# Performance work log

Measured on AMD Instinct MI355X. Metric: run time of the kernel, lower is better.

## Reference

```python
import jax, jax.numpy as jnp
import numpy as np
import math

B, N, A = 4, 2048, 128          # batch, natoms, neighbor_num
EMB = [1, 25, 50, 100]           # embedding net sizes (input dim 1 = S_Rij)
M = EMB[-1]
FIT = [16 * M, 240, 240, 240, 1] # fitting net sizes
RMIN, RMAX = 5.8, 6.0


def setup_inputs() -> dict:
    key = jax.random.key(0)
    ks = jax.random.split(key, 16)
    inp = {}
    inp["image_dR"] = jax.random.normal(ks[0], (B, N, A, 3), jnp.float32)
    inp["list_neigh"] = jax.random.randint(ks[1], (B, N, A), 0, N)
    ki = 2
    for i in range(3):
        inp[f"We{i}"] = jax.random.normal(ks[ki], (EMB[i], EMB[i + 1]), jnp.float32) / np.sqrt(EMB[i]).astype(np.float32)
        inp[f"be{i}"] = jnp.zeros((EMB[i + 1],), jnp.float32)
        ki += 1
    for i in range(4):
        inp[f"Wf{i}"] = jax.random.normal(ks[ki], (FIT[i], FIT[i + 1]), jnp.float32) / np.sqrt(FIT[i]).astype(np.float32)
        inp[f"bf{i}"] = jnp.zeros((FIT[i + 1],), jnp.float32)
        ki += 1
    return inp


def _forward(image_dR, list_neigh, We0, be0, We1, be1, We2, be2,
             Wf0, bf0, Wf1, bf1, Wf2, bf2, Wf3, bf3):
    # NOTE: the original assigns Rij = sqrt(dR2) then immediately overwrites
    # Rij = dR2, so all smooth/division math uses the SQUARED distance.
    Rij = jnp.sum(image_dR * image_dR, axis=-1)  # [B,N,A]
    mask = list_neigh > 0

    # smooth(): 1/x for valid & x<rmin; cosine taper for rmin<=x<rmax (unmasked,
    # exactly as in source); 0 elsewhere.
    mask_min = Rij < RMIN
    safe = jnp.where(Rij > 0, Rij, 1.0)
    s_inv = 1.0 / safe
    s_cos = 0.5 * jnp.cos(math.pi * (Rij - RMIN) / (RMAX - RMIN)) + 0.5
    S_Rij = jnp.where(mask & mask_min, s_inv,
                      jnp.where((~mask_min) & (Rij < RMAX), s_cos, 0.0))

    # The Python loop breaks at the first non-positive neighbor index, so only
    # the valid PREFIX of each neighbor list gets directional components.
    prefix = jnp.cumprod(mask.astype(jnp.int32), axis=-1).astype(bool)  # [B,N,A]
    coords = jnp.where(prefix[..., None], (S_Rij * s_inv)[..., None] * image_dR, 0.0)
    Ri = jnp.concatenate([S_Rij[..., None], coords], axis=-1)  # [B,N,A,4]

    # embedding net: S_Rij -> M channels (tanh MLP)
    h = S_Rij[..., None]
    h = jnp.tanh(h @ We0 + be0)
    h = jnp.tanh(h @ We1 + be1)
    G = jnp.tanh(h @ We2 + be2)  # [B,N,A,M]

    # tmpA = G[...,:16]^T @ Ri : [B,N,16,4];  tmpB = Ri^T @ G : [B,N,4,M]
    tmpA = jnp.einsum('bnam,bnac->bnmc', G[..., :16], Ri)
    tmpB = jnp.einsum('bnac,bnaM->bncM', Ri, G)
    DR = jnp.einsum('bnmc,bncM->bnmM', tmpA, tmpB).reshape(Ri.shape[0], Ri.shape[1], -1)  # [B,N,16*M]

    # fitting net
    h = jnp.tanh(DR @ Wf0 + bf0)
    h = jnp.tanh(h @ Wf1 + bf1)
    h = jnp.tanh(h @ Wf2 + bf2)
    Ei = h @ Wf3 + bf3          # [B,N,1]
    Etot = jnp.sum(Ei, axis=1)  # [B,1]
    return Etot, Ei


def reference(image_dR, list_neigh, We0, be0, We1, be1, We2, be2,
              Wf0, bf0, Wf1, bf1, Wf2, bf2, Wf3, bf3):
    return _forward(image_dR, list_neigh, We0, be0, We1, be1, We2, be2,
                    Wf0, bf0, Wf1, bf1, Wf2, bf2, Wf3, bf3)
```

## Files before the change

### kernel.cpp

```cpp
#include <hip/hip_runtime.h>
#include <hip/hip_bf16.h>
#include <math.h>
#include <stdint.h>

#define NB 4
#define NN 2048
#define NA 128
#define NK 2048
#define RMINF 5.8f
#define RMAXF 6.0f
#define PI_OVER_DR 15.707963267948966f

typedef __attribute__((ext_vector_type(8))) short short8v;
typedef __attribute__((ext_vector_type(4))) float f32x4;

__device__ __forceinline__ float fast_tanh(float x)
{
    x = fminf(fmaxf(x, -15.f), 15.f);
    float e = __expf(2.f * x);
    float r = __builtin_amdgcn_rcpf(e + 1.f);
    return fmaf(-2.f, r, 1.f);
}

__device__ __forceinline__ uint16_t bf16_of(float x)
{
    __hip_bfloat16 b = __float2bfloat16(x);
    return *(uint16_t*)&b;
}

__device__ __forceinline__ float bf16_to_f(uint16_t v)
{
    union { uint32_t u; float f; } c; c.u = ((uint32_t)v) << 16; return c.f;
}

__device__ __forceinline__ size_t packed_off(int r, int k, int Ktot)
{
    return ((size_t)((r >> 4) * (Ktot >> 5) + (k >> 5)) << 9)
         + (((r & 15) + (((k >> 3) & 3) << 4)) << 3) + (k & 7);
}

__device__ __forceinline__ float knot_S(int knot)
{
    float uu = (float)knot / (float)NK;
    return (knot == NK) ? 1e8f : uu / (1.f - uu);
}

__global__ void prep_h2_kernel(
    const float* __restrict__ We0, const float* __restrict__ be0,
    const float* __restrict__ We1, const float* __restrict__ be1,
    float* __restrict__ H2)
{
    int idx = blockIdx.x * 256 + threadIdx.x;
    if (idx >= (NK + 1) * 50) return;
    int knot = idx / 50, j = idx - knot * 50;
    float S = knot_S(knot);
    float acc = be1[j];
    #pragma unroll
    for (int k = 0; k < 25; ++k) {
        float h1k = fast_tanh(fmaf(S, We0[k], be0[k]));
        acc = fmaf(h1k, We1[k * 50 + j], acc);
    }
    H2[idx] = fast_tanh(acc);
}

__global__ void prep_tbl_kernel(
    const float* __restrict__ H2,
    const float* __restrict__ We2, const float* __restrict__ be2,
    float* __restrict__ TBL)
{
    int idx = blockIdx.x * 256 + threadIdx.x;
    if (idx >= (NK + 1) * 100) return;
    int knot = idx / 100, j = idx - knot * 100;
    const float* h2 = H2 + knot * 50;
    float acc = be2[j];
    #pragma unroll
    for (int k = 0; k < 50; ++k)
        acc = fmaf(h2[k], We2[k * 100 + j], acc);
    TBL[idx] = fast_tanh(acc);
}

__global__ void prep_wt_kernel(const float* __restrict__ W,
                               uint16_t* __restrict__ Whi,
                               uint16_t* __restrict__ Wlo,
                               int K, int KP)
{
    int idx = blockIdx.x * 256 + threadIdx.x;
    if (idx < 256 * KP) {
        int colN = idx / KP, k = idx - colN * KP;
        float v = (colN < 240 && k < K) ? W[k * 240 + colN] : 0.f;
        uint16_t hi = bf16_of(v);
        size_t off = packed_off(colN, k, KP);
        Whi[off] = hi;
        Wlo[off] = bf16_of(v - bf16_to_f(hi));
    }
}

__global__ __launch_bounds__(256) void desc_kernel(
    const float* __restrict__ dR, const int* __restrict__ neigh,
    const float* __restrict__ TBL,
    uint16_t* __restrict__ DRhi)
{
    const int bid = blockIdx.x;
    const int atom = (bid & 7) * 1024 + (bid >> 3);
    const int t = threadIdx.x;

    __shared__ float4 RiSh[128];
    __shared__ float2 IFSh[128];
    __shared__ float  tmpPart[8][4][100];
    __shared__ float  tmpBf[4][100];
    __shared__ unsigned long long balls[2];

    float x = 0.f, y = 0.f, z = 0.f, S = 0.f, s_inv = 1.f;
    if (t < 128) {
        const int base = atom * NA;
        x = dR[(base + t) * 3 + 0];
        y = dR[(base + t) * 3 + 1];
        z = dR[(base + t) * 3 + 2];
        int nb = neigh[base + t];
        float Rij = x * x + y * y + z * z;
        bool mask = nb > 0;
        bool mask_min = Rij < RMINF;
        float safe = (Rij > 0.f) ? Rij : 1.f;
        s_inv = 1.f / safe;
        float s_cos = 0.5f * cosf((Rij - RMINF) * PI_OVER_DR) + 0.5f;
        S = (mask && mask_min) ? s_inv
          : ((!mask_min && Rij < RMAXF) ? s_cos : 0.f);
        unsigned long long bal = __ballot(mask);
        if ((t & 63) == 0) balls[t >> 6] = bal;
    }
    __syncthreads();

    if (t < 128) {
        unsigned long long nb0 = ~balls[0], nb1 = ~balls[1];
        int firstBad;
        if (nb0)       firstBad = __ffsll((long long)nb0) - 1;
        else if (nb1)  firstBad = 64 + __ffsll((long long)nb1) - 1;
        else           firstBad = 128;
        float f = (t < firstBad) ? (S * s_inv) : 0.f;
        RiSh[t] = make_float4(S, f * x, f * y, f * z);
        float uu = S / (1.f + S);
        float pos = fminf(uu * (float)NK, (float)NK - 0.001f);
        float fi = floorf(pos);
        IFSh[t] = make_float2(pos - fi, __int_as_float((int)fi * 100));
    }
    __syncthreads();

    const int aq = t >> 5;
    const int jq = t & 31;
    if (jq < 25) {
        const float* TBLq = TBL + jq * 4;
        const int a0 = aq * 16;
        float acc00 = 0.f, acc01 = 0.f, acc02 = 0.f, acc03 = 0.f;
        float acc10 = 0.f, acc11 = 0.f, acc12 = 0.f, acc13 = 0.f;
        float acc20 = 0.f, acc21 = 0.f, acc22 = 0.f, acc23 = 0.f;
        float acc30 = 0.f, acc31 = 0.f, acc32 = 0.f, acc33 = 0.f;

        float2 ifv = IFSh[a0];
        float  cf  = ifv.x;
        int    ia  = __float_as_int(ifv.y);
        float4 t0  = *(const float4*)(TBLq + ia);
        float4 t1  = *(const float4*)(TBLq + ia + 100);
        #pragma unroll
        for (int i = 0; i < 16; ++i) {
            float g0 = fmaf(cf, t1.x - t0.x, t0.x);
            float g1 = fmaf(cf, t1.y - t0.y, t0.y);
            float g2 = fmaf(cf, t1.z - t0.z, t0.z);
            float g3 = fmaf(cf, t1.w - t0.w, t0.w);
            if (i + 1 < 16) {
                float2 nx = IFSh[a0 + i + 1];
                cf = nx.x;
                int ian = __float_as_int(nx.y);
                t0 = *(const float4*)(TBLq + ian);
                t1 = *(const float4*)(TBLq + ian + 100);
            }
            float4 cri = RiSh[a0 + i];
            acc00 = fmaf(cri.x, g0, acc00); acc01 = fmaf(cri.x, g1, acc01);
            acc02 = fmaf(cri.x, g2, acc02); acc03 = fmaf(cri.x, g3, acc03);
            acc10 = fmaf(cri.y, g0, acc10); acc11 = fmaf(cri.y, g1, acc11);
            acc12 = fmaf(cri.y, g2, acc12); acc13 = fmaf(cri.y, g3, acc13);
            acc20 = fmaf(cri.z, g0, acc20); acc21 = fmaf(cri.z, g1, acc21);
            acc22 = fmaf(cri.z, g2, acc22); acc23 = fmaf(cri.z, g3, acc23);
            acc30 = fmaf(cri.w, g0, acc30); acc31 = fmaf(cri.w, g1, acc31);
            acc32 = fmaf(cri.w, g2, acc32); acc33 = fmaf(cri.w, g3, acc33);
        }
        *(float4*)&tmpPart[aq][0][jq * 4] = make_float4(acc00, acc01, acc02, acc03);
        *(float4*)&tmpPart[aq][1][jq * 4] = make_float4(acc10, acc11, acc12, acc13);
        *(float4*)&tmpPart[aq][2][jq * 4] = make_float4(acc20, acc21, acc22, acc23);
        *(float4*)&tmpPart[aq][3][jq * 4] = make_float4(acc30, acc31, acc32, acc33);
    }
    __syncthreads();

    for (int idx = t; idx < 400; idx += 256) {
        int c = idx / 100, j = idx - c * 100;
        float s = tmpPart[0][c][j] + tmpPart[1][c][j]
                + tmpPart[2][c][j] + tmpPart[3][c][j]
                + tmpPart[4][c][j] + tmpPart[5][c][j]
                + tmpPart[6][c][j] + tmpPart[7][c][j];
        tmpBf[c][j] = s;
    }
    __syncthreads();

    const int half = t >> 7;
    const int u = t & 127;
    if (u < 100) {
        float b0 = tmpBf[0][u];
        float b1 = tmpBf[1][u];
        float b2 = tmpBf[2][u];
        float b3 = tmpBf[3][u];
        const int i0 = half * 8;
        #pragma unroll
        for (int ii = 0; ii < 8; ++ii) {
            int i = i0 + ii;
            float v = tmpBf[0][i] * b0 + tmpBf[1][i] * b1
                    + tmpBf[2][i] * b2 + tmpBf[3][i] * b3;
            DRhi[packed_off(atom, i * 100 + u, 1600)] = bf16_of(v);
        }
    }
}

template<int KP, int KSPLIT>
__global__ __launch_bounds__(256, 4) void gemm_part(
    const uint16_t* __restrict__ Ahi,
    const uint16_t* __restrict__ Wthi, const uint16_t* __restrict__ Wtlo,
    float* __restrict__ Part)
{
    constexpr int KT = KP >> 5;
    constexpr int STEPS = KT / KSPLIT;
    const int tid = threadIdx.x;
    const int wid = tid >> 6, lane = tid & 63;
    const int mg = wid >> 1, ng = wid & 1;
    const int mt0 = blockIdx.x * 4 + mg * 2;
    const int nt0 = blockIdx.y * 4 + ng * 2;
    const int kt0 = blockIdx.z * STEPS;

    const size_t aB0 = ((size_t)(mt0 + 0) * KT + kt0) * 512 + lane * 8;
    const size_t aB1 = ((size_t)(mt0 + 1) * KT + kt0) * 512 + lane * 8;
    const size_t bB0 = ((size_t)(nt0 + 0) * KT + kt0) * 512 + lane * 8;
    const size_t bB1 = ((size_t)(nt0 + 1) * KT + kt0) * 512 + lane * 8;

    f32x4 acc[2][2];
    #pragma unroll
    for (int m = 0; m < 2; ++m)
        #pragma unroll
        for (int n = 0; n < 2; ++n) acc[m][n] = (f32x4){0.f, 0.f, 0.f, 0.f};

    short8v f[2][6];

#define LOADSET(B, S) do {                                       \
        f[B][0] = *(const short8v*)(Ahi  + aB0 + (S) * 512);     \
        f[B][1] = *(const short8v*)(Ahi  + aB1 + (S) * 512);     \
        f[B][2] = *(const short8v*)(Wthi + bB0 + (S) * 512);     \
        f[B][3] = *(const short8v*)(Wthi + bB1 + (S) * 512);     \
        f[B][4] = *(const short8v*)(Wtlo + bB0 + (S) * 512);     \
        f[B][5] = *(const short8v*)(Wtlo + bB1 + (S) * 512);     \
    } while (0)

    LOADSET(0, 0);
    #pragma unroll
    for (int s = 0; s < STEPS; ++s) {
        const int b = s & 1;
        if (s + 1 < STEPS) LOADSET(b ^ 1, s + 1);
        #pragma unroll
        for (int m = 0; m < 2; ++m)
            #pragma unroll
            for (int n = 0; n < 2; ++n) {
                acc[m][n] = __builtin_amdgcn_mfma_f32_16x16x32_bf16(f[b][m], f[b][2 + n], acc[m][n], 0, 0, 0);
                acc[m][n] = __builtin_amdgcn_mfma_f32_16x16x32_bf16(f[b][m], f[b][4 + n], acc[m][n], 0, 0, 0);
            }
    }
#undef LOADSET

    const int ar = lane & 15, kg = lane >> 4;
    float* pp = Part + (size_t)blockIdx.z * (8192 * 256);
    #pragma unroll
    for (int m = 0; m < 2; ++m)
        #pragma unroll
        for (int n = 0; n < 2; ++n)
            #pragma unroll
            for (int r = 0; r < 4; ++r)
                pp[(size_t)((mt0 + m) * 16 + kg * 4 + r) * 256 + (nt0 + n) * 16 + ar] = acc[m][n][r];
}

template<int KP>
__global__ __launch_bounds__(256, 4) void gemm_fused(
    const uint16_t* __restrict__ Ahi, const uint16_t* __restrict__ Alo,
    const uint16_t* __restrict__ Wthi, const uint16_t* __restrict__ Wtlo,
    const float* __restrict__ bias,
    uint16_t* __restrict__ Ohi, uint16_t* __restrict__ Olo)
{
    constexpr int KT = KP >> 5;
    constexpr int STEPS = KT;
    const int tid = threadIdx.x;
    const int wid = tid >> 6, lane = tid & 63;
    const int mg = wid >> 1, ng = wid & 1;
    const int mt0 = blockIdx.x * 4 + mg * 2;
    const int nt0 = blockIdx.y * 4 + ng * 2;

    const size_t aB0 = ((size_t)(mt0 + 0) * KT) * 512 + lane * 8;
    const size_t aB1 = ((size_t)(mt0 + 1) * KT) * 512 + lane * 8;
    const size_t bB0 = ((size_t)(nt0 + 0) * KT) * 512 + lane * 8;
    const size_t bB1 = ((size_t)(nt0 + 1) * KT) * 512 + lane * 8;

    f32x4 acc[2][2];
    #pragma unroll
    for (int m = 0; m < 2; ++m)
        #pragma unroll
        for (int n = 0; n < 2; ++n) acc[m][n] = (f32x4){0.f, 0.f, 0.f, 0.f};

    short8v f[2][8];

#define LOADSET(B, S) do {                                       \
        f[B][0] = *(const short8v*)(Ahi  + aB0 + (S) * 512);     \
        f[B][1] = *(const short8v*)(Ahi  + aB1 + (S) * 512);     \
        f[B][2] = *(const short8v*)(Alo  + aB0 + (S) * 512);     \
        f[B][3] = *(const short8v*)(Alo  + aB1 + (S) * 512);     \
        f[B][4] = *(const short8v*)(Wthi + bB0 + (S) * 512);     \
        f[B][5] = *(const short8v*)(Wthi + bB1 + (S) * 512);     \
        f[B][6] = *(const short8v*)(Wtlo + bB0 + (S) * 512);     \
        f[B][7] = *(const short8v*)(Wtlo + bB1 + (S) * 512);     \
    } while (0)

    LOADSET(0, 0);
    #pragma unroll
    for (int s = 0; s < STEPS; ++s) {
        const int b = s & 1;
        if (s + 1 < STEPS) LOADSET(b ^ 1, s + 1);
        #pragma unroll
        for (int m = 0; m < 2; ++m)
            #pragma unroll
            for (int n = 0; n < 2; ++n) {
                acc[m][n] = __builtin_amdgcn_mfma_f32_16x16x32_bf16(f[b][m],     f[b][4 + n], acc[m][n], 0, 0, 0);
                acc[m][n] = __builtin_amdgcn_mfma_f32_16x16x32_bf16(f[b][m],     f[b][6 + n], acc[m][n], 0, 0, 0);
                acc[m][n] = __builtin_amdgcn_mfma_f32_16x16x32_bf16(f[b][2 + m], f[b][4 + n], acc[m][n], 0, 0, 0);
            }
    }
#undef LOADSET

    const int ar = lane & 15, kg = lane >> 4;
    #pragma unroll
    for (int n = 0; n < 2; ++n) {
        int col = (nt0 + n) * 16 + ar;
        bool valid = col < 240;
        float bv = valid ? bias[col] : 0.f;
        #pragma unroll
        for (int m = 0; m < 2; ++m) {
            #pragma unroll
            for (int r = 0; r < 4; ++r) {
                int row = (mt0 + m) * 16 + kg * 4 + r;
                float v = valid ? fast_tanh(acc[m][n][r] + bv) : 0.f;
                uint16_t hi = bf16_of(v);
                size_t off = packed_off(row, col, 256);
                Ohi[off] = hi;
                Olo[off] = bf16_of(v - bf16_to_f(hi));
            }
        }
    }
}

__global__ __launch_bounds__(256) void gemm_epi(
    const float* __restrict__ Part, const float* __restrict__ bias,
    uint16_t* __restrict__ Ohi, uint16_t* __restrict__ Olo)
{
    int g = (blockIdx.x & 7) * 256 + (blockIdx.x >> 3);
    int idx0 = g * 1024 + threadIdx.x;
    #pragma unroll
    for (int it = 0; it < 4; ++it) {
        int idx = idx0 + it * 256;
        int col = idx & 255;
        int row = idx >> 8;
        float s = Part[idx] + Part[idx + 8192 * 256];
        float v = (col < 240) ? fast_tanh(s + bias[col]) : 0.f;
        uint16_t hi = bf16_of(v);
        size_t off = packed_off(row, col, 256);
        Ohi[off] = hi;
        Olo[off] = bf16_of(v - bf16_to_f(hi));
    }
}

__global__ __launch_bounds__(256) void final_dot_kernel(
    const uint16_t* __restrict__ Hhi, const uint16_t* __restrict__ Hlo,
    const float* __restrict__ Wf3, const float* __restrict__ bf3,
    float* __restrict__ out)
{
    int wave = threadIdx.x >> 6, lane = threadIdx.x & 63;
    int atom = blockIdx.x * 4 + wave;
    float v = 0.f;
    if (lane < 60) {
        size_t off = packed_off(atom, lane * 4, 256);
        ushort4 h4 = *(const ushort4*)(Hhi + off);
        ushort4 l4 = *(const ushort4*)(Hlo + off);
        float4 w = *(const float4*)&Wf3[lane * 4];
        v = (bf16_to_f(h4.x) + bf16_to_f(l4.x)) * w.x
          + (bf16_to_f(h4.y) + bf16_to_f(l4.y)) * w.y
          + (bf16_to_f(h4.z) + bf16_to_f(l4.z)) * w.z
          + (bf16_to_f(h4.w) + bf16_to_f(l4.w)) * w.w;
    }
    #pragma unroll
    for (int off = 32; off; off >>= 1) v += __shfl_down(v, off, 64);
    if (lane == 0) out[4 + atom] = v + bf3[0];
}

__global__ __launch_bounds__(256) void etot_kernel(float* __restrict__ out)
{
    __shared__ float red[256];
    int b = blockIdx.x, t = threadIdx.x;
    float s = 0.f;
    for (int i = t; i < NN; i += 256) s += out[4 + b * NN + i];
    red[t] = s;
    __syncthreads();
    for (int w = 128; w; w >>= 1) {
        if (t < w) red[t] += red[t + w];
        __syncthreads();
    }
    if (t == 0) out[b] = red[0];
}

extern "C" void kernel_launch(void* const* d_in, const int* in_sizes, int n_in,
                              void* d_out, int out_size, void* d_ws, size_t ws_size,
                              hipStream_t stream)
{
    const float* dR    = (const float*)d_in[0];
    const int*   neigh = (const int*)d_in[1];
    const float* We0   = (const float*)d_in[2];
    const float* be0   = (const float*)d_in[3];
    const float* We1   = (const float*)d_in[4];
    const float* be1   = (const float*)d_in[5];
    const float* We2   = (const float*)d_in[6];
    const float* be2   = (const float*)d_in[7];
    const float* Wf0   = (const float*)d_in[8];
    const float* bf0   = (const float*)d_in[9];
    const float* Wf1   = (const float*)d_in[10];
    const float* bf1   = (const float*)d_in[11];
    const float* Wf2   = (const float*)d_in[12];
    const float* bf2   = (const float*)d_in[13];
    const float* Wf3   = (const float*)d_in[14];
    const float* bf3   = (const float*)d_in[15];
    float* out = (float*)d_out;

    char* ws = (char*)d_ws;
    uint16_t* Wt0hi  = (uint16_t*)(ws + 32768);
    uint16_t* Wt0lo  = (uint16_t*)(ws + 851968);
    uint16_t* Wt1hi  = (uint16_t*)(ws + 1671168);
    uint16_t* Wt1lo  = (uint16_t*)(ws + 1802240);
    uint16_t* Wt2hi  = (uint16_t*)(ws + 1933312);
    uint16_t* Wt2lo  = (uint16_t*)(ws + 2064384);
    uint16_t* DRhi   = (uint16_t*)(ws + 2195456);
    uint16_t* hAhi   = (uint16_t*)(ws + 54624256);
    uint16_t* hAlo   = (uint16_t*)(ws + 58818560);
    uint16_t* hBhi   = (uint16_t*)(ws + 63012864);
    uint16_t* hBlo   = (uint16_t*)(ws + 67207168);
    float* H2  = (float*)(ws + 54624256);
    float* TBL = (float*)(ws + 63012864);
    float* Part1 = (float*)(ws + 63012864);

    prep_h2_kernel<<<401, 256, 0, stream>>>(We0, be0, We1, be1, H2);
    prep_tbl_kernel<<<801, 256, 0, stream>>>(H2, We2, be2, TBL);
    prep_wt_kernel<<<1600, 256, 0, stream>>>(Wf0, Wt0hi, Wt0lo, 1600, 1600);
    prep_wt_kernel<<<256, 256, 0, stream>>>(Wf1, Wt1hi, Wt1lo, 240, 256);
    prep_wt_kernel<<<256, 256, 0, stream>>>(Wf2, Wt2hi, Wt2lo, 240, 256);

    desc_kernel<<<NB * NN, 256, 0, stream>>>(dR, neigh, TBL, DRhi);

    gemm_part<1600, 2><<<dim3(128, 4, 2), 256, 0, stream>>>(DRhi, Wt0hi, Wt0lo, Part1);
    gemm_epi<<<2048, 256, 0, stream>>>(Part1, bf0, hAhi, hAlo);
    gemm_fused<256><<<dim3(128, 4), 256, 0, stream>>>(hAhi, hAlo, Wt1hi, Wt1lo, bf1, hBhi, hBlo);
    gemm_fused<256><<<dim3(128, 4), 256, 0, stream>>>(hBhi, hBlo, Wt2hi, Wt2lo, bf2, hAhi, hAlo);

    final_dot_kernel<<<NB * NN / 4, 256, 0, stream>>>(hAhi, hAlo, Wf3, bf3, out);
    etot_kernel<<<NB, 256, 0, stream>>>(out);
}
```

Measured before the change: 133.8 us.

## Fuse GEMM epilogues, final dot product and weight prep into fewer kernels

The three weight-prep launches become one kernel that picks its matrix from the block index. The first GEMM drops its 2-way split-K with a float partial buffer and separate epilogue kernel, and instead applies bias, tanh and the hi/lo bf16 split in registers. The last hidden GEMM is fused with the Wf3 dot product through wave shuffles, writing per-slice partial energies that one small kernel reduces into Ei and Etot. This removes launches and the intermediate global traffic, but the first GEMM now has half as many blocks, each running a K-loop twice as long, which lowers parallelism.

```diff
diff --git a/kernel.cpp b/kernel.cpp
--- a/kernel.cpp
+++ b/kernel.cpp
@@ -79,12 +79,9 @@
     TBL[idx] = fast_tanh(acc);
 }
 
-__global__ void prep_wt_kernel(const float* __restrict__ W,
-                               uint16_t* __restrict__ Whi,
-                               uint16_t* __restrict__ Wlo,
-                               int K, int KP)
-{
-    int idx = blockIdx.x * 256 + threadIdx.x;
+__device__ __forceinline__ void wt_one(const float* W, uint16_t* Whi, uint16_t* Wlo,
+                                       int K, int KP, int idx)
+{
     if (idx < 256 * KP) {
         int colN = idx / KP, k = idx - colN * KP;
         float v = (colN < 240 && k < K) ? W[k * 240 + colN] : 0.f;
@@ -93,6 +90,19 @@
         Whi[off] = hi;
         Wlo[off] = bf16_of(v - bf16_to_f(hi));
     }
+}
+
+__global__ void prep_wt_all_kernel(
+    const float* __restrict__ Wf0, const float* __restrict__ Wf1,
+    const float* __restrict__ Wf2,
+    uint16_t* __restrict__ W0hi, uint16_t* __restrict__ W0lo,
+    uint16_t* __restrict__ W1hi, uint16_t* __restrict__ W1lo,
+    uint16_t* __restrict__ W2hi, uint16_t* __restrict__ W2lo)
+{
+    int bid = blockIdx.x, t = threadIdx.x;
+    if (bid < 1600)       wt_one(Wf0, W0hi, W0lo, 1600, 1600, bid * 256 + t);
+    else if (bid < 1856)  wt_one(Wf1, W1hi, W1lo, 240, 256, (bid - 1600) * 256 + t);
+    else                  wt_one(Wf2, W2hi, W2lo, 240, 256, (bid - 1856) * 256 + t);
 }
 
 __global__ __launch_bounds__(256) void desc_kernel(
@@ -218,25 +228,24 @@
     }
 }
 
-template<int KP, int KSPLIT>
-__global__ __launch_bounds__(256, 4) void gemm_part(
+template<int KP>
+__global__ __launch_bounds__(256, 4) void gemm1_fused(
     const uint16_t* __restrict__ Ahi,
     const uint16_t* __restrict__ Wthi, const uint16_t* __restrict__ Wtlo,
-    float* __restrict__ Part)
+    const float* __restrict__ bias,
+    uint16_t* __restrict__ Ohi, uint16_t* __restrict__ Olo)
 {
     constexpr int KT = KP >> 5;
-    constexpr int STEPS = KT / KSPLIT;
     const int tid = threadIdx.x;
     const int wid = tid >> 6, lane = tid & 63;
     const int mg = wid >> 1, ng = wid & 1;
     const int mt0 = blockIdx.x * 4 + mg * 2;
     const int nt0 = blockIdx.y * 4 + ng * 2;
-    const int kt0 = blockIdx.z * STEPS;
-
-    const size_t aB0 = ((size_t)(mt0 + 0) * KT + kt0) * 512 + lane * 8;
-    const size_t aB1 = ((size_t)(mt0 + 1) * KT + kt0) * 512 + lane * 8;
-    const size_t bB0 = ((size_t)(nt0 + 0) * KT + kt0) * 512 + lane * 8;
-    const size_t bB1 = ((size_t)(nt0 + 1) * KT + kt0) * 512 + lane * 8;
+
+    const size_t aB0 = ((size_t)(mt0 + 0) * KT) * 512 + lane * 8;
+    const size_t aB1 = ((size_t)(mt0 + 1) * KT) * 512 + lane * 8;
+    const size_t bB0 = ((size_t)(nt0 + 0) * KT) * 512 + lane * 8;
+    const size_t bB1 = ((size_t)(nt0 + 1) * KT) * 512 + lane * 8;
 
     f32x4 acc[2][2];
     #pragma unroll
@@ -257,9 +266,9 @@
 
     LOADSET(0, 0);
     #pragma unroll
-    for (int s = 0; s < STEPS; ++s) {
+    for (int s = 0; s < KT; ++s) {
         const int b = s & 1;
-        if (s + 1 < STEPS) LOADSET(b ^ 1, s + 1);
+        if (s + 1 < KT) LOADSET(b ^ 1, s + 1);
         #pragma unroll
         for (int m = 0; m < 2; ++m)
             #pragma unroll
@@ -271,14 +280,24 @@
 #undef LOADSET
 
     const int ar = lane & 15, kg = lane >> 4;
-    float* pp = Part + (size_t)blockIdx.z * (8192 * 256);
-    #pragma unroll
-    for (int m = 0; m < 2; ++m)
-        #pragma unroll
-        for (int n = 0; n < 2; ++n)
-            #pragma unroll
-            for (int r = 0; r < 4; ++r)
-                pp[(size_t)((mt0 + m) * 16 + kg * 4 + r) * 256 + (nt0 + n) * 16 + ar] = acc[m][n][r];
+    #pragma unroll
+    for (int n = 0; n < 2; ++n) {
+        int col = (nt0 + n) * 16 + ar;
+        bool valid = col < 240;
+        float bv = valid ? bias[col] : 0.f;
+        #pragma unroll
+        for (int m = 0; m < 2; ++m) {
+            #pragma unroll
+            for (int r = 0; r < 4; ++r) {
+                int row = (mt0 + m) * 16 + kg * 4 + r;
+                float v = valid ? fast_tanh(acc[m][n][r] + bv) : 0.f;
+                uint16_t hi = bf16_of(v);
+                size_t off = packed_off(row, col, 256);
+                Ohi[off] = hi;
+                Olo[off] = bf16_of(v - bf16_to_f(hi));
+            }
+        }
+    }
 }
 
 template<int KP>
@@ -289,7 +308,6 @@
     uint16_t* __restrict__ Ohi, uint16_t* __restrict__ Olo)
 {
     constexpr int KT = KP >> 5;
-    constexpr int STEPS = KT;
     const int tid = threadIdx.x;
     const int wid = tid >> 6, lane = tid & 63;
     const int mg = wid >> 1, ng = wid & 1;
@@ -322,9 +340,9 @@
 
     LOADSET(0, 0);
     #pragma unroll
-    for (int s = 0; s < STEPS; ++s) {
+    for (int s = 0; s < KT; ++s) {
         const int b = s & 1;
-        if (s + 1 < STEPS) LOADSET(b ^ 1, s + 1);
+        if (s + 1 < KT) LOADSET(b ^ 1, s + 1);
         #pragma unroll
         for (int m = 0; m < 2; ++m)
             #pragma unroll
@@ -357,55 +375,119 @@
     }
 }
 
-__global__ __launch_bounds__(256) void gemm_epi(
-    const float* __restrict__ Part, const float* __restrict__ bias,
-    uint16_t* __restrict__ Ohi, uint16_t* __restrict__ Olo)
-{
-    int g = (blockIdx.x & 7) * 256 + (blockIdx.x >> 3);
-    int idx0 = g * 1024 + threadIdx.x;
-    #pragma unroll
-    for (int it = 0; it < 4; ++it) {
-        int idx = idx0 + it * 256;
-        int col = idx & 255;
-        int row = idx >> 8;
-        float s = Part[idx] + Part[idx + 8192 * 256];
-        float v = (col < 240) ? fast_tanh(s + bias[col]) : 0.f;
-        uint16_t hi = bf16_of(v);
-        size_t off = packed_off(row, col, 256);
-        Ohi[off] = hi;
-        Olo[off] = bf16_of(v - bf16_to_f(hi));
-    }
-}
-
-__global__ __launch_bounds__(256) void final_dot_kernel(
-    const uint16_t* __restrict__ Hhi, const uint16_t* __restrict__ Hlo,
-    const float* __restrict__ Wf3, const float* __restrict__ bf3,
+template<int KP>
+__global__ __launch_bounds__(256, 4) void gemm_fused_dot(
+    const uint16_t* __restrict__ Ahi, const uint16_t* __restrict__ Alo,
+    const uint16_t* __restrict__ Wthi, const uint16_t* __restrict__ Wtlo,
+    const float* __restrict__ bias, const float* __restrict__ Wf3,
+    float* __restrict__ EiPart)
+{
+    constexpr int KT = KP >> 5;
+    const int tid = threadIdx.x;
+    const int wid = tid >> 6, lane = tid & 63;
+    const int mg = wid >> 1, ng = wid & 1;
+    const int mt0 = blockIdx.x * 4 + mg * 2;
+    const int nt0 = blockIdx.y * 4 + ng * 2;
+
+    const size_t aB0 = ((size_t)(mt0 + 0) * KT) * 512 + lane * 8;
+    const size_t aB1 = ((size_t)(mt0 + 1) * KT) * 512 + lane * 8;
+    const size_t bB0 = ((size_t)(nt0 + 0) * KT) * 512 + lane * 8;
+    const size_t bB1 = ((size_t)(nt0 + 1) * KT) * 512 + lane * 8;
+
+    f32x4 acc[2][2];
+    #pragma unroll
+    for (int m = 0; m < 2; ++m)
+        #pragma unroll
+        for (int n = 0; n < 2; ++n) acc[m][n] = (f32x4){0.f, 0.f, 0.f, 0.f};
+
+    short8v f[2][8];
+
+#define LOADSET(B, S) do {                                       \
+        f[B][0] = *(const short8v*)(Ahi  + aB0 + (S) * 512);     \
+        f[B][1] = *(const short8v*)(Ahi  + aB1 + (S) * 512);     \
+        f[B][2] = *(const short8v*)(Alo  + aB0 + (S) * 512);     \
+        f[B][3] = *(const short8v*)(Alo  + aB1 + (S) * 512);     \
+        f[B][4] = *(const short8v*)(Wthi + bB0 + (S) * 512);     \
+        f[B][5] = *(const short8v*)(Wthi + bB1 + (S) * 512);     \
+        f[B][6] = *(const short8v*)(Wtlo + bB0 + (S) * 512);     \
+        f[B][7] = *(const short8v*)(Wtlo + bB1 + (S) * 512);     \
+    } while (0)
+
+    LOADSET(0, 0);
+    #pragma unroll
+    for (int s = 0; s < KT; ++s) {
+        const int b = s & 1;
+        if (s + 1 < KT) LOADSET(b ^ 1, s + 1);
+        #pragma unroll
+        for (int m = 0; m < 2; ++m)
+            #pragma unroll
+            for (int n = 0; n < 2; ++n) {
+                acc[m][n] = __builtin_amdgcn_mfma_f32_16x16x32_bf16(f[b][m],     f[b][4 + n], acc[m][n], 0, 0, 0);
+                acc[m][n] = __builtin_amdgcn_mfma_f32_16x16x32_bf16(f[b][m],     f[b][6 + n], acc[m][n], 0, 0, 0);
+                acc[m][n] = __builtin_amdgcn_mfma_f32_16x16x32_bf16(f[b][2 + m], f[b][4 + n], acc[m][n], 0, 0, 0);
+            }
+    }
+#undef LOADSET
+
+    const int ar = lane & 15, kg = lane >> 4;
+    float p[2][4];
+    #pragma unroll
+    for (int m = 0; m < 2; ++m)
+        #pragma unroll
+        for (int r = 0; r < 4; ++r) p[m][r] = 0.f;
+
+    #pragma unroll
+    for (int n = 0; n < 2; ++n) {
+        int col = (nt0 + n) * 16 + ar;
+        bool valid = col < 240;
+        float bv = valid ? bias[col] : 0.f;
+        float w3 = valid ? Wf3[col] : 0.f;
+        #pragma unroll
+        for (int m = 0; m < 2; ++m) {
+            #pragma unroll
+            for (int r = 0; r < 4; ++r) {
+                float v = valid ? fast_tanh(acc[m][n][r] + bv) : 0.f;
+                p[m][r] = fmaf(v, w3, p[m][r]);
+            }
+        }
+    }
+    #pragma unroll
+    for (int m = 0; m < 2; ++m)
+        #pragma unroll
+        for (int r = 0; r < 4; ++r) {
+            p[m][r] += __shfl_xor(p[m][r], 1, 64);
+            p[m][r] += __shfl_xor(p[m][r], 2, 64);
+            p[m][r] += __shfl_xor(p[m][r], 4, 64);
+            p[m][r] += __shfl_xor(p[m][r], 8, 64);
+        }
+    if (ar == 0) {
+        const int slice = blockIdx.y * 2 + ng;
+        #pragma unroll
+        for (int m = 0; m < 2; ++m)
+            #pragma unroll
+            for (int r = 0; r < 4; ++r) {
+                int row = (mt0 + m) * 16 + kg * 4 + r;
+                EiPart[(size_t)slice * 8192 + row] = p[m][r];
+            }
+    }
+}
+
+__global__ __launch_bounds__(256) void ei_etot_kernel(
+    const float* __restrict__ EiPart, const float* __restrict__ bf3,
     float* __restrict__ out)
-{
-    int wave = threadIdx.x >> 6, lane = threadIdx.x & 63;
-    int atom = blockIdx.x * 4 + wave;
-    float v = 0.f;
-    if (lane < 60) {
-        size_t off = packed_off(atom, lane * 4, 256);
-        ushort4 h4 = *(const ushort4*)(Hhi + off);
-        ushort4 l4 = *(const ushort4*)(Hlo + off);
-        float4 w = *(const float4*)&Wf3[lane * 4];
-        v = (bf16_to_f(h4.x) + bf16_to_f(l4.x)) * w.x
-          + (bf16_to_f(h4.y) + bf16_to_f(l4.y)) * w.y
-          + (bf16_to_f(h4.z) + bf16_to_f(l4.z)) * w.z
-          + (bf16_to_f(h4.w) + bf16_to_f(l4.w)) * w.w;
-    }
-    #pragma unroll
-    for (int off = 32; off; off >>= 1) v += __shfl_down(v, off, 64);
-    if (lane == 0) out[4 + atom] = v + bf3[0];
-}
-
-__global__ __launch_bounds__(256) void etot_kernel(float* __restrict__ out)
 {
     __shared__ float red[256];
     int b = blockIdx.x, t = threadIdx.x;
+    float b3 = bf3[0];
     float s = 0.f;
-    for (int i = t; i < NN; i += 256) s += out[4 + b * NN + i];
+    for (int i = t; i < NN; i += 256) {
+        int atom = b * NN + i;
+        float e = b3;
+        #pragma unroll
+        for (int z = 0; z < 8; ++z) e += EiPart[(size_t)z * 8192 + atom];
+        out[4 + atom] = e;
+        s += e;
+    }
     red[t] = s;
     __syncthreads();
     for (int w = 128; w; w >>= 1) {
@@ -449,23 +531,21 @@
     uint16_t* hAlo   = (uint16_t*)(ws + 58818560);
     uint16_t* hBhi   = (uint16_t*)(ws + 63012864);
     uint16_t* hBlo   = (uint16_t*)(ws + 67207168);
+    float*    EiPart = (float*)(ws + 71401472);
     float* H2  = (float*)(ws + 54624256);
     float* TBL = (float*)(ws + 63012864);
-    float* Part1 = (float*)(ws + 63012864);
 
     prep_h2_kernel<<<401, 256, 0, stream>>>(We0, be0, We1, be1, H2);
     prep_tbl_kernel<<<801, 256, 0, stream>>>(H2, We2, be2, TBL);
-    prep_wt_kernel<<<1600, 256, 0, stream>>>(Wf0, Wt0hi, Wt0lo, 1600, 1600);
-    prep_wt_kernel<<<256, 256, 0, stream>>>(Wf1, Wt1hi, Wt1lo, 240, 256);
-    prep_wt_kernel<<<256, 256, 0, stream>>>(Wf2, Wt2hi, Wt2lo, 240, 256);
+    prep_wt_all_kernel<<<2112, 256, 0, stream>>>(Wf0, Wf1, Wf2,
+                                                 Wt0hi, Wt0lo, Wt1hi, Wt1lo,
+                                                 Wt2hi, Wt2lo);
 
     desc_kernel<<<NB * NN, 256, 0, stream>>>(dR, neigh, TBL, DRhi);
 
-    gemm_part<1600, 2><<<dim3(128, 4, 2), 256, 0, stream>>>(DRhi, Wt0hi, Wt0lo, Part1);
-    gemm_epi<<<2048, 256, 0, stream>>>(Part1, bf0, hAhi, hAlo);
+    gemm1_fused<1600><<<dim3(128, 4), 256, 0, stream>>>(DRhi, Wt0hi, Wt0lo, bf0, hAhi, hAlo);
     gemm_fused<256><<<dim3(128, 4), 256, 0, stream>>>(hAhi, hAlo, Wt1hi, Wt1lo, bf1, hBhi, hBlo);
-    gemm_fused<256><<<dim3(128, 4), 256, 0, stream>>>(hBhi, hBlo, Wt2hi, Wt2lo, bf2, hAhi, hAlo);
-
-    final_dot_kernel<<<NB * NN / 4, 256, 0, stream>>>(hAhi, hAlo, Wf3, bf3, out);
-    etot_kernel<<<NB, 256, 0, stream>>>(out);
-}
+    gemm_fused_dot<256><<<dim3(128, 4), 256, 0, stream>>>(hBhi, hBlo, Wt2hi, Wt2lo, bf2, Wf3, EiPart);
+
+    ei_etot_kernel<<<NB, 256, 0, stream>>>(EiPart, bf3, out);
+}
```

Measured after the change: 121.0 us. -9.6%, faster.
